# Kernel optimization log

Hardware: AMD Instinct MI355X
Metric: run time of the kernel (lower is better)

Reference implementation:

```python
import jax, jax.numpy as jnp
import numpy as np

B, T, D, H = 2, 2048, 1024, 16
DK = D // H


def setup_inputs() -> dict:
    key = jax.random.key(0)
    ks = jax.random.split(key, 12)
    s = 0.02
    return {
        "query": jax.random.normal(ks[0], (B, T, D), jnp.float32),
        "key": jax.random.normal(ks[1], (B, T, D), jnp.float32),
        "value": jax.random.normal(ks[2], (B, T, D), jnp.float32),
        "mask": jax.random.randint(ks[3], (B, T), 0, 2) != 0,  # True = keep
        "Wq": jax.random.normal(ks[4], (D, D), jnp.float32) * s,
        "bq": jnp.zeros((D,), jnp.float32),
        "Wk": jax.random.normal(ks[5], (D, D), jnp.float32) * s,
        "bk": jnp.zeros((D,), jnp.float32),
        "Wv": jax.random.normal(ks[6], (D, D), jnp.float32) * s,
        "bv": jnp.zeros((D,), jnp.float32),
        "Wo": jax.random.normal(ks[7], (D, D), jnp.float32) * s,
        "bo": jnp.zeros((D,), jnp.float32),
    }


def _split_heads(x):
    # [B, S, D] -> [B, H, S, DK]
    b, s, _ = x.shape
    return x.reshape(b, s, H, DK).transpose(0, 2, 1, 3)


def reference(query, key, value, mask, Wq, bq, Wk, bk, Wv, bv, Wo, bo):
    # torch Linear: y = x @ W.T + b
    q = _split_heads(query @ Wq.T + bq)   # [B,H,T,DK]
    k = _split_heads(key @ Wk.T + bk)     # [B,H,S,DK]
    v = _split_heads(value @ Wv.T + bv)   # [B,H,S,DK]
    scale = 1.0 / np.sqrt(DK).astype(np.float32)
    scores = jnp.einsum('bhtd,bhsd->bhts', q, k) * scale  # [B,H,T,S]
    # key-padding mask [B,S] -> broadcast [B,1,1,S], True = keep
    scores = jnp.where(mask[:, None, None, :], scores, -jnp.inf)
    attn = jax.nn.softmax(scores, axis=-1)
    out = jnp.einsum('bhts,bhsd->bhtd', attn, v)           # [B,H,T,DK]
    out = out.transpose(0, 2, 1, 3).reshape(query.shape[0], -1, D)
    return out @ Wo.T + bo
```

## Files before the change

kernel.cpp:

```cpp
#include <hip/hip_runtime.h>
#include <stdint.h>

#define B_SZ 2
#define T_SEQ 2048
#define DMODEL 1024
#define NHEAD 16
#define DKH 64
#define M_ROWS (B_SZ * T_SEQ)

#define LDT 72

#define INP_E  4194304u
#define W_E    1048576u

typedef __bf16 bf16x8 __attribute__((ext_vector_type(8)));
typedef float  f32x4  __attribute__((ext_vector_type(4)));

__device__ __forceinline__ unsigned short f2bf(float f) {
    unsigned u = __builtin_bit_cast(unsigned, f);
    u += 0x7fffu + ((u >> 16) & 1u);
    return (unsigned short)(u >> 16);
}
__device__ __forceinline__ uint4 cvt8(const float* p) {
    float4 f0 = *(const float4*)p, f1 = *(const float4*)(p + 4);
    uint4 r;
    r.x = (unsigned)f2bf(f0.x) | ((unsigned)f2bf(f0.y) << 16);
    r.y = (unsigned)f2bf(f0.z) | ((unsigned)f2bf(f0.w) << 16);
    r.z = (unsigned)f2bf(f1.x) | ((unsigned)f2bf(f1.y) << 16);
    r.w = (unsigned)f2bf(f1.z) | ((unsigned)f2bf(f1.w) << 16);
    return r;
}

__device__ __forceinline__ void async16(const unsigned short* g, unsigned short* l) {
    __builtin_amdgcn_global_load_lds(
        (const __attribute__((address_space(1))) void*)g,
        (__attribute__((address_space(3))) void*)l, 16, 0, 0);
}

__global__ __launch_bounds__(256) void cvt_all(
    const float* __restrict__ q, const float* __restrict__ k, const float* __restrict__ v,
    const float* __restrict__ wq, const float* __restrict__ wk,
    const float* __restrict__ wv, const float* __restrict__ wo,
    unsigned short* __restrict__ wsb)
{
    int blk = blockIdx.x;
    const float* src; unsigned short* dst; int lb;
    if      (blk < 2048) { src = q;  dst = wsb;                       lb = blk; }
    else if (blk < 4096) { src = k;  dst = wsb + INP_E;               lb = blk - 2048; }
    else if (blk < 6144) { src = v;  dst = wsb + 2 * INP_E;           lb = blk - 4096; }
    else if (blk < 6656) { src = wq; dst = wsb + 3 * INP_E;           lb = blk - 6144; }
    else if (blk < 7168) { src = wk; dst = wsb + 3 * INP_E + W_E;     lb = blk - 6656; }
    else if (blk < 7680) { src = wv; dst = wsb + 3 * INP_E + 2 * W_E; lb = blk - 7168; }
    else                 { src = wo; dst = wsb + 3 * INP_E + 3 * W_E; lb = blk - 7680; }
    size_t i = ((size_t)lb * 256 + threadIdx.x) * 8;
    *(uint4*)&dst[i] = cvt8(src + i);
}

template<int C_MODE>
__device__ __forceinline__ void gemm_core(
    const unsigned short* __restrict__ A, const unsigned short* __restrict__ W,
    const float* __restrict__ bias, void* __restrict__ C,
    int N, int K, int bx, int by,
    unsigned short* sA, unsigned short* sB)
{
    const int tid  = threadIdx.x;
    const int wave = tid >> 6, lane = tid & 63;
    const int quad = lane >> 4, l15 = lane & 15;
    const int m0 = by * 128, n0 = bx * 128;
    const int wm = (wave & 1) * 64, wn = (wave >> 1) * 64;

    f32x4 acc[4][4] = {};

    for (int k0 = 0; k0 < K; k0 += 64) {
        __syncthreads();
        #pragma unroll
        for (int i = 0; i < 4; i++) {
            int c   = tid + 256 * i;
            int row = c >> 3;
            int gk  = ((c & 7) ^ (row & 7)) * 8;
            int sb  = (wave * 64 + 256 * i) * 8;
            async16(&A[(size_t)(m0 + row) * K + k0 + gk], sA + sb);
            async16(&W[(size_t)(n0 + row) * K + k0 + gk], sB + sb);
        }
        __syncthreads();
        #pragma unroll
        for (int ks = 0; ks < 2; ks++) {
            const int sw = l15 & 7;
            bf16x8 af[4], bfv[4];
            #pragma unroll
            for (int mt = 0; mt < 4; mt++)
                af[mt] = *(const bf16x8*)&sA[(wm + mt * 16 + l15) * 64 +
                                             (((ks * 4 + quad) ^ sw) * 8)];
            #pragma unroll
            for (int nt = 0; nt < 4; nt++)
                bfv[nt] = *(const bf16x8*)&sB[(wn + nt * 16 + l15) * 64 +
                                              (((ks * 4 + quad) ^ sw) * 8)];
            #pragma unroll
            for (int mt = 0; mt < 4; mt++)
                #pragma unroll
                for (int nt = 0; nt < 4; nt++)
                    acc[mt][nt] = __builtin_amdgcn_mfma_f32_16x16x32_bf16(
                        af[mt], bfv[nt], acc[mt][nt], 0, 0, 0);
        }
    }

    if (C_MODE == 2) {
        #pragma unroll
        for (int mt = 0; mt < 4; mt++) {
            #pragma unroll
            for (int r = 0; r < 4; r++) {
                int m = m0 + wm + mt * 16 + quad * 4 + r;
                float bm = bias[m];
                #pragma unroll
                for (int nt = 0; nt < 4; nt++) {
                    int n = n0 + wn + nt * 16 + l15;
                    int bb = n >> 11, t = n & 2047;
                    ((unsigned short*)C)[((size_t)bb * 1024 + m) * 2048 + t] =
                        f2bf(acc[mt][nt][r] + bm);
                }
            }
        }
    } else {
        #pragma unroll
        for (int nt = 0; nt < 4; nt++) {
            int n = n0 + wn + nt * 16 + l15;
            float bv = bias[n];
            #pragma unroll
            for (int mt = 0; mt < 4; mt++) {
                #pragma unroll
                for (int r = 0; r < 4; r++) {
                    int m = m0 + wm + mt * 16 + quad * 4 + r;
                    float val = acc[mt][nt][r] + bv;
                    if (C_MODE == 1) ((float*)C)[(size_t)m * N + n] = val;
                    else ((unsigned short*)C)[(size_t)m * N + n] = f2bf(val);
                }
            }
        }
    }
}

__global__ __launch_bounds__(256) void gemm_qkv(
    const unsigned short* __restrict__ Qb, const unsigned short* __restrict__ Kb,
    const unsigned short* __restrict__ Vb,
    const unsigned short* __restrict__ Wqb, const unsigned short* __restrict__ Wkb,
    const unsigned short* __restrict__ Wvb,
    const float* __restrict__ bq, const float* __restrict__ bk, const float* __restrict__ bv,
    unsigned short* __restrict__ Qp, unsigned short* __restrict__ Kp,
    unsigned short* __restrict__ Vt)
{
    __shared__ __align__(16) unsigned short sA[128 * 64];
    __shared__ __align__(16) unsigned short sB[128 * 64];
    const int z = blockIdx.z, id = blockIdx.x;
    if (z < 2) {
        gemm_core<0>(z ? Kb : Qb, z ? Wkb : Wqb, z ? bk : bq, z ? Kp : Qp,
                     DMODEL, DMODEL, id & 7, id >> 3, sA, sB);
    } else {
        gemm_core<2>(Wvb, Vb, bv, Vt, M_ROWS, DMODEL, id & 31, id >> 5, sA, sB);
    }
}

__global__ __launch_bounds__(256) void gemm_o(
    const unsigned short* __restrict__ AO, const unsigned short* __restrict__ Wob,
    const float* __restrict__ bo, float* __restrict__ out)
{
    __shared__ __align__(16) unsigned short sA[128 * 64];
    __shared__ __align__(16) unsigned short sB[128 * 64];
    const int id = blockIdx.x;
    gemm_core<1>(AO, Wob, bo, out, DMODEL, DMODEL, id & 7, id >> 3, sA, sB);
}

template<int A_BF16, int W_BF16, int C_MODE>
__global__ __launch_bounds__(256) void gemm_bt_cvt(
    const void* __restrict__ A_, const void* __restrict__ W_,
    const float* __restrict__ bias, void* __restrict__ C_,
    int M, int N, int K)
{
    __shared__ __align__(16) unsigned short sA[128 * LDT];
    __shared__ __align__(16) unsigned short sB[128 * LDT];
    const int tid  = threadIdx.x;
    const int wave = tid >> 6, lane = tid & 63;
    const int quad = lane >> 4, l15 = lane & 15;
    const int m0 = blockIdx.y * 128, n0 = blockIdx.x * 128;
    const int wm = (wave & 1) * 64, wn = (wave >> 1) * 64;
    f32x4 acc[4][4] = {};
    for (int k0 = 0; k0 < K; k0 += 64) {
        __syncthreads();
        #pragma unroll
        for (int i = 0; i < 4; i++) {
            int c = tid + 256 * i;
            int row = c >> 3, koff = (c & 7) * 8;
            if (A_BF16)
                *(uint4*)&sA[row * LDT + koff] =
                    *(const uint4*)&((const unsigned short*)A_)[(size_t)(m0 + row) * K + k0 + koff];
            else
                *(uint4*)&sA[row * LDT + koff] =
                    cvt8((const float*)A_ + (size_t)(m0 + row) * K + k0 + koff);
            if (W_BF16)
                *(uint4*)&sB[row * LDT + koff] =
                    *(const uint4*)&((const unsigned short*)W_)[(size_t)(n0 + row) * K + k0 + koff];
            else
                *(uint4*)&sB[row * LDT + koff] =
                    cvt8((const float*)W_ + (size_t)(n0 + row) * K + k0 + koff);
        }
        __syncthreads();
        #pragma unroll
        for (int ks = 0; ks < 2; ks++) {
            bf16x8 af[4], bfr[4];
            #pragma unroll
            for (int mt = 0; mt < 4; mt++)
                af[mt] = *(const bf16x8*)&sA[(wm + mt * 16 + l15) * LDT + ks * 32 + quad * 8];
            #pragma unroll
            for (int nt = 0; nt < 4; nt++)
                bfr[nt] = *(const bf16x8*)&sB[(wn + nt * 16 + l15) * LDT + ks * 32 + quad * 8];
            #pragma unroll
            for (int mt = 0; mt < 4; mt++)
                #pragma unroll
                for (int nt = 0; nt < 4; nt++)
                    acc[mt][nt] = __builtin_amdgcn_mfma_f32_16x16x32_bf16(
                        af[mt], bfr[nt], acc[mt][nt], 0, 0, 0);
        }
    }
    if (C_MODE == 2) {
        #pragma unroll
        for (int mt = 0; mt < 4; mt++)
            #pragma unroll
            for (int r = 0; r < 4; r++) {
                int m = m0 + wm + mt * 16 + quad * 4 + r;
                float bm = bias[m];
                #pragma unroll
                for (int nt = 0; nt < 4; nt++) {
                    int n = n0 + wn + nt * 16 + l15;
                    int bb = n >> 11, t = n & 2047;
                    ((unsigned short*)C_)[((size_t)bb * 1024 + m) * 2048 + t] =
                        f2bf(acc[mt][nt][r] + bm);
                }
            }
    } else {
        #pragma unroll
        for (int nt = 0; nt < 4; nt++) {
            int n = n0 + wn + nt * 16 + l15;
            float bv = bias[n];
            #pragma unroll
            for (int mt = 0; mt < 4; mt++)
                #pragma unroll
                for (int r = 0; r < 4; r++) {
                    int m = m0 + wm + mt * 16 + quad * 4 + r;
                    float val = acc[mt][nt][r] + bv;
                    if (C_MODE == 1) ((float*)C_)[(size_t)m * N + n] = val;
                    else ((unsigned short*)C_)[(size_t)m * N + n] = f2bf(val);
                }
        }
    }
}

__global__ __launch_bounds__(256) void attn_kernel(
    const unsigned short* __restrict__ Qp,
    const unsigned short* __restrict__ Kp,
    const unsigned short* __restrict__ Vt,
    const int* __restrict__ maskp,
    unsigned short* __restrict__ Op)
{
    __shared__ __align__(16) unsigned short sK[64 * LDT];
    __shared__ __align__(16) unsigned short sV[64 * LDT];
    __shared__ __align__(16) unsigned short sP[4 * 16 * LDT];
    __shared__ float smask[64];

    const int tid  = threadIdx.x;
    const int wave = tid >> 6, lane = tid & 63;
    const int quad = lane >> 4, l15 = lane & 15;
    const int qblk = blockIdx.x, h = blockIdx.y, b = blockIdx.z;

    const float SCL2 = 0.125f * 1.44269504089f;
    const float MNEG = -30000.f;

    const int qrow = qblk * 64 + wave * 16 + l15;
    const unsigned short* qptr = Qp + (size_t)(b * T_SEQ + qrow) * DMODEL + h * DKH + quad * 8;
    const bf16x8 aq0 = *(const bf16x8*)qptr;
    const bf16x8 aq1 = *(const bf16x8*)(qptr + 32);

    f32x4 O[4] = {};
    float l_r[4] = {0.f, 0.f, 0.f, 0.f};

    unsigned short* sPw = sP + wave * 16 * LDT;
    const unsigned short* VtB = Vt + (size_t)b * DMODEL * T_SEQ + (size_t)h * DKH * T_SEQ;

    for (int s0 = 0; s0 < T_SEQ; s0 += 64) {
        __syncthreads();
        #pragma unroll
        for (int i = 0; i < 2; i++) {
            int c = tid + 256 * i;
            int row = c >> 3, off = (c & 7) * 8;
            *(uint4*)&sK[row * LDT + off] =
                *(const uint4*)&Kp[(size_t)(b * T_SEQ + s0 + row) * DMODEL + h * DKH + off];
            *(uint4*)&sV[row * LDT + off] =
                *(const uint4*)&VtB[(size_t)row * T_SEQ + s0 + off];
        }
        if (tid < 64)
            smask[tid] = maskp[b * T_SEQ + s0 + tid] ? 0.f : MNEG;
        __syncthreads();

        f32x4 S[4];
        #pragma unroll
        for (int nt = 0; nt < 4; nt++) {
            const unsigned short* kb = &sK[(nt * 16 + l15) * LDT + quad * 8];
            f32x4 z = {};
            z = __builtin_amdgcn_mfma_f32_16x16x32_bf16(aq0, *(const bf16x8*)kb, z, 0, 0, 0);
            z = __builtin_amdgcn_mfma_f32_16x16x32_bf16(aq1, *(const bf16x8*)(kb + 32), z, 0, 0, 0);
            S[nt] = z;
        }

        #pragma unroll
        for (int nt = 0; nt < 4; nt++) {
            float madd = smask[nt * 16 + l15];
            #pragma unroll
            for (int r = 0; r < 4; r++) {
                float p = __builtin_amdgcn_exp2f(S[nt][r] * SCL2 + madd);
                l_r[r] += p;
                unsigned u = __builtin_bit_cast(unsigned, p) + 0x8000u;
                sPw[(quad * 4 + r) * LDT + nt * 16 + l15] = (unsigned short)(u >> 16);
            }
        }
        __syncthreads();

        const bf16x8 ap0 = *(const bf16x8*)&sPw[l15 * LDT + quad * 8];
        const bf16x8 ap1 = *(const bf16x8*)&sPw[l15 * LDT + 32 + quad * 8];
        #pragma unroll
        for (int nt = 0; nt < 4; nt++) {
            const unsigned short* vb = &sV[(nt * 16 + l15) * LDT + quad * 8];
            O[nt] = __builtin_amdgcn_mfma_f32_16x16x32_bf16(ap0, *(const bf16x8*)vb, O[nt], 0, 0, 0);
            O[nt] = __builtin_amdgcn_mfma_f32_16x16x32_bf16(ap1, *(const bf16x8*)(vb + 32), O[nt], 0, 0, 0);
        }
    }

    #pragma unroll
    for (int r = 0; r < 4; r++) {
        float l = l_r[r];
        l += __shfl_xor(l, 1);
        l += __shfl_xor(l, 2);
        l += __shfl_xor(l, 4);
        l += __shfl_xor(l, 8);
        l_r[r] = 1.0f / fmaxf(l, 1e-30f);
    }
    #pragma unroll
    for (int nt = 0; nt < 4; nt++) {
        #pragma unroll
        for (int r = 0; r < 4; r++) {
            int q = qblk * 64 + wave * 16 + quad * 4 + r;
            Op[(size_t)(b * T_SEQ + q) * DMODEL + h * DKH + nt * 16 + l15] =
                f2bf(O[nt][r] * l_r[r]);
        }
    }
}

extern "C" void kernel_launch(void* const* d_in, const int* in_sizes, int n_in,
                              void* d_out, int out_size, void* d_ws, size_t ws_size,
                              hipStream_t stream)
{
    const float* q  = (const float*)d_in[0];
    const float* k  = (const float*)d_in[1];
    const float* v  = (const float*)d_in[2];
    const int*   mk = (const int*)d_in[3];
    const float* Wq = (const float*)d_in[4];
    const float* bq = (const float*)d_in[5];
    const float* Wk = (const float*)d_in[6];
    const float* bk = (const float*)d_in[7];
    const float* Wv = (const float*)d_in[8];
    const float* bv = (const float*)d_in[9];
    const float* Wo = (const float*)d_in[10];
    const float* bo = (const float*)d_in[11];
    float* out = (float*)d_out;

    unsigned short* wsb = (unsigned short*)d_ws;
    const dim3 gA(T_SEQ / 64, NHEAD, B_SZ);

    if (ws_size >= (size_t)64 * 1024 * 1024) {
        unsigned short* Qb  = wsb;
        unsigned short* Kb  = wsb + INP_E;
        unsigned short* Vb  = wsb + 2 * INP_E;
        unsigned short* Wqb = wsb + 3 * INP_E;
        unsigned short* Wkb = wsb + 3 * INP_E + W_E;
        unsigned short* Wvb = wsb + 3 * INP_E + 2 * W_E;
        unsigned short* Wob = wsb + 3 * INP_E + 3 * W_E;
        unsigned short* Qp  = wsb + 4 * INP_E;
        unsigned short* Kp  = wsb + 5 * INP_E;
        unsigned short* Vt  = wsb + 6 * INP_E;
        unsigned short* AO  = wsb + 7 * INP_E;

        cvt_all<<<8192, 256, 0, stream>>>(q, k, v, Wq, Wk, Wv, Wo, wsb);
        gemm_qkv<<<dim3(256, 1, 3), 256, 0, stream>>>(
            Qb, Kb, Vb, Wqb, Wkb, Wvb, bq, bk, bv, Qp, Kp, Vt);
        attn_kernel<<<gA, 256, 0, stream>>>(Qp, Kp, Vt, mk, AO);
        gemm_o<<<dim3(256, 1, 1), 256, 0, stream>>>(AO, Wob, bo, out);
    } else {
        unsigned short* Qp = wsb;
        unsigned short* Kp = wsb + INP_E;
        unsigned short* Vt = wsb + 2 * INP_E;
        unsigned short* AO = wsb + 3 * INP_E;
        const dim3 gN(DMODEL / 128, M_ROWS / 128);
        const dim3 gV(M_ROWS / 128, DMODEL / 128);
        gemm_bt_cvt<0, 0, 0><<<gN, 256, 0, stream>>>(q, Wq, bq, Qp, M_ROWS, DMODEL, DMODEL);
        gemm_bt_cvt<0, 0, 0><<<gN, 256, 0, stream>>>(k, Wk, bk, Kp, M_ROWS, DMODEL, DMODEL);
        gemm_bt_cvt<0, 0, 2><<<gV, 256, 0, stream>>>(Wv, v, bv, Vt, DMODEL, M_ROWS, DMODEL);
        attn_kernel<<<gA, 256, 0, stream>>>(Qp, Kp, Vt, mk, AO);
        gemm_bt_cvt<1, 0, 1><<<gN, 256, 0, stream>>>(AO, Wo, bo, out, M_ROWS, DMODEL, DMODEL);
    }
}
```

Baseline: 256.9 us.

## Enlarge attention key tile with register prefetch; halve output GEMM M-tile

Result: slower. 348.3 us (+35.6%).

```diff
diff --git a/kernel.cpp b/kernel.cpp
--- a/kernel.cpp
+++ b/kernel.cpp
@@ -9,6 +9,7 @@
 #define M_ROWS (B_SZ * T_SEQ)
 
 #define LDT 72
+#define LDP 136
 
 #define INP_E  4194304u
 #define W_E    1048576u
@@ -56,7 +57,7 @@
     *(uint4*)&dst[i] = cvt8(src + i);
 }
 
-template<int C_MODE>
+template<int C_MODE, int MT>
 __device__ __forceinline__ void gemm_core(
     const unsigned short* __restrict__ A, const unsigned short* __restrict__ W,
     const float* __restrict__ bias, void* __restrict__ C,
@@ -66,29 +67,37 @@
     const int tid  = threadIdx.x;
     const int wave = tid >> 6, lane = tid & 63;
     const int quad = lane >> 4, l15 = lane & 15;
-    const int m0 = by * 128, n0 = bx * 128;
-    const int wm = (wave & 1) * 64, wn = (wave >> 1) * 64;
-
-    f32x4 acc[4][4] = {};
+    const int TM = MT * 32;
+    const int m0 = by * TM, n0 = bx * 128;
+    const int wm = (wave & 1) * (MT * 16), wn = (wave >> 1) * 64;
+
+    f32x4 acc[MT][4] = {};
 
     for (int k0 = 0; k0 < K; k0 += 64) {
         __syncthreads();
+        #pragma unroll
+        for (int i = 0; i < MT; i++) {
+            int c   = tid + 256 * i;
+            int row = c >> 3;
+            int gk  = ((c & 7) ^ (row & 7)) * 8;
+            int sb  = (wave * 64 + 256 * i) * 8;
+            async16(&A[(size_t)(m0 + row) * K + k0 + gk], sA + sb);
+        }
         #pragma unroll
         for (int i = 0; i < 4; i++) {
             int c   = tid + 256 * i;
             int row = c >> 3;
             int gk  = ((c & 7) ^ (row & 7)) * 8;
             int sb  = (wave * 64 + 256 * i) * 8;
-            async16(&A[(size_t)(m0 + row) * K + k0 + gk], sA + sb);
             async16(&W[(size_t)(n0 + row) * K + k0 + gk], sB + sb);
         }
         __syncthreads();
+        const int sw = l15 & 7;
         #pragma unroll
         for (int ks = 0; ks < 2; ks++) {
-            const int sw = l15 & 7;
-            bf16x8 af[4], bfv[4];
-            #pragma unroll
-            for (int mt = 0; mt < 4; mt++)
+            bf16x8 af[MT], bfv[4];
+            #pragma unroll
+            for (int mt = 0; mt < MT; mt++)
                 af[mt] = *(const bf16x8*)&sA[(wm + mt * 16 + l15) * 64 +
                                              (((ks * 4 + quad) ^ sw) * 8)];
             #pragma unroll
@@ -96,7 +105,7 @@
                 bfv[nt] = *(const bf16x8*)&sB[(wn + nt * 16 + l15) * 64 +
                                               (((ks * 4 + quad) ^ sw) * 8)];
             #pragma unroll
-            for (int mt = 0; mt < 4; mt++)
+            for (int mt = 0; mt < MT; mt++)
                 #pragma unroll
                 for (int nt = 0; nt < 4; nt++)
                     acc[mt][nt] = __builtin_amdgcn_mfma_f32_16x16x32_bf16(
@@ -106,7 +115,7 @@
 
     if (C_MODE == 2) {
         #pragma unroll
-        for (int mt = 0; mt < 4; mt++) {
+        for (int mt = 0; mt < MT; mt++) {
             #pragma unroll
             for (int r = 0; r < 4; r++) {
                 int m = m0 + wm + mt * 16 + quad * 4 + r;
@@ -126,7 +135,7 @@
             int n = n0 + wn + nt * 16 + l15;
             float bv = bias[n];
             #pragma unroll
-            for (int mt = 0; mt < 4; mt++) {
+            for (int mt = 0; mt < MT; mt++) {
                 #pragma unroll
                 for (int r = 0; r < 4; r++) {
                     int m = m0 + wm + mt * 16 + quad * 4 + r;
@@ -152,10 +161,10 @@
     __shared__ __align__(16) unsigned short sB[128 * 64];
     const int z = blockIdx.z, id = blockIdx.x;
     if (z < 2) {
-        gemm_core<0>(z ? Kb : Qb, z ? Wkb : Wqb, z ? bk : bq, z ? Kp : Qp,
-                     DMODEL, DMODEL, id & 7, id >> 3, sA, sB);
+        gemm_core<0, 4>(z ? Kb : Qb, z ? Wkb : Wqb, z ? bk : bq, z ? Kp : Qp,
+                        DMODEL, DMODEL, id & 7, id >> 3, sA, sB);
     } else {
-        gemm_core<2>(Wvb, Vb, bv, Vt, M_ROWS, DMODEL, id & 31, id >> 5, sA, sB);
+        gemm_core<2, 4>(Wvb, Vb, bv, Vt, M_ROWS, DMODEL, id & 31, id >> 5, sA, sB);
     }
 }
 
@@ -163,10 +172,131 @@
     const unsigned short* __restrict__ AO, const unsigned short* __restrict__ Wob,
     const float* __restrict__ bo, float* __restrict__ out)
 {
-    __shared__ __align__(16) unsigned short sA[128 * 64];
+    __shared__ __align__(16) unsigned short sA[64 * 64];
     __shared__ __align__(16) unsigned short sB[128 * 64];
     const int id = blockIdx.x;
-    gemm_core<1>(AO, Wob, bo, out, DMODEL, DMODEL, id & 7, id >> 3, sA, sB);
+    gemm_core<1, 2>(AO, Wob, bo, out, DMODEL, DMODEL, id & 7, id >> 3, sA, sB);
+}
+
+__global__ __launch_bounds__(256) void attn_kernel(
+    const unsigned short* __restrict__ Qp,
+    const unsigned short* __restrict__ Kp,
+    const unsigned short* __restrict__ Vt,
+    const int* __restrict__ maskp,
+    unsigned short* __restrict__ Op)
+{
+    __shared__ __align__(16) unsigned short sK[128 * LDT];
+    __shared__ __align__(16) unsigned short sV[64 * LDP];
+    __shared__ __align__(16) unsigned short sP[4 * 16 * LDP];
+    __shared__ float smask[128];
+
+    const int tid  = threadIdx.x;
+    const int wave = tid >> 6, lane = tid & 63;
+    const int quad = lane >> 4, l15 = lane & 15;
+    const int qblk = blockIdx.x, h = blockIdx.y, b = blockIdx.z;
+
+    const float SCL2 = 0.125f * 1.44269504089f;
+    const float MNEG = -30000.f;
+
+    const int qrow = qblk * 64 + wave * 16 + l15;
+    const unsigned short* qptr = Qp + (size_t)(b * T_SEQ + qrow) * DMODEL + h * DKH + quad * 8;
+    const bf16x8 aq0 = *(const bf16x8*)qptr;
+    const bf16x8 aq1 = *(const bf16x8*)(qptr + 32);
+
+    const unsigned short* Kb_ = Kp + (size_t)b * T_SEQ * DMODEL + h * DKH;
+    const unsigned short* VtB = Vt + ((size_t)b * DMODEL + h * DKH) * T_SEQ;
+
+    f32x4 O[4] = {};
+    float l_r[4] = {0.f, 0.f, 0.f, 0.f};
+    unsigned short* sPw = sP + wave * 16 * LDP;
+
+    int krow[4], koff[4], vrow[4], voff[4];
+    #pragma unroll
+    for (int i = 0; i < 4; i++) {
+        int c = tid + 256 * i;
+        krow[i] = c >> 3;  koff[i] = (c & 7) * 8;
+        vrow[i] = c >> 4;  voff[i] = (c & 15) * 8;
+    }
+
+    uint4 kr[4], vr[4]; int mreg = 0;
+    #pragma unroll
+    for (int i = 0; i < 4; i++) {
+        kr[i] = *(const uint4*)&Kb_[(size_t)krow[i] * DMODEL + koff[i]];
+        vr[i] = *(const uint4*)&VtB[(size_t)vrow[i] * T_SEQ + voff[i]];
+    }
+    if (tid < 128) mreg = maskp[b * T_SEQ + tid];
+
+    for (int it = 0; it < T_SEQ / 128; it++) {
+        const int s0 = it * 128;
+        __syncthreads();
+        #pragma unroll
+        for (int i = 0; i < 4; i++) {
+            *(uint4*)&sK[krow[i] * LDT + koff[i]] = kr[i];
+            *(uint4*)&sV[vrow[i] * LDP + voff[i]] = vr[i];
+        }
+        if (tid < 128) smask[tid] = mreg ? 0.f : MNEG;
+        __syncthreads();
+
+        const int sn = (s0 + 128) & (T_SEQ - 1);
+        #pragma unroll
+        for (int i = 0; i < 4; i++) {
+            kr[i] = *(const uint4*)&Kb_[(size_t)(sn + krow[i]) * DMODEL + koff[i]];
+            vr[i] = *(const uint4*)&VtB[(size_t)vrow[i] * T_SEQ + sn + voff[i]];
+        }
+        if (tid < 128) mreg = maskp[b * T_SEQ + sn + tid];
+
+        f32x4 S[8];
+        #pragma unroll
+        for (int nt = 0; nt < 8; nt++) {
+            const unsigned short* kb = &sK[(nt * 16 + l15) * LDT + quad * 8];
+            f32x4 z = {};
+            z = __builtin_amdgcn_mfma_f32_16x16x32_bf16(aq0, *(const bf16x8*)kb, z, 0, 0, 0);
+            z = __builtin_amdgcn_mfma_f32_16x16x32_bf16(aq1, *(const bf16x8*)(kb + 32), z, 0, 0, 0);
+            S[nt] = z;
+        }
+
+        #pragma unroll
+        for (int nt = 0; nt < 8; nt++) {
+            float madd = smask[nt * 16 + l15];
+            #pragma unroll
+            for (int r = 0; r < 4; r++) {
+                float p = __builtin_amdgcn_exp2f(fmaf(S[nt][r], SCL2, madd));
+                l_r[r] += p;
+                unsigned u = __builtin_bit_cast(unsigned, p) + 0x8000u;
+                sPw[(quad * 4 + r) * LDP + nt * 16 + l15] = (unsigned short)(u >> 16);
+            }
+        }
+        __syncthreads();
+
+        #pragma unroll
+        for (int ksc = 0; ksc < 4; ksc++) {
+            const bf16x8 ap = *(const bf16x8*)&sPw[l15 * LDP + ksc * 32 + quad * 8];
+            #pragma unroll
+            for (int nt = 0; nt < 4; nt++) {
+                const unsigned short* vb = &sV[(nt * 16 + l15) * LDP + ksc * 32 + quad * 8];
+                O[nt] = __builtin_amdgcn_mfma_f32_16x16x32_bf16(ap, *(const bf16x8*)vb, O[nt], 0, 0, 0);
+            }
+        }
+    }
+
+    #pragma unroll
+    for (int r = 0; r < 4; r++) {
+        float l = l_r[r];
+        l += __shfl_xor(l, 1);
+        l += __shfl_xor(l, 2);
+        l += __shfl_xor(l, 4);
+        l += __shfl_xor(l, 8);
+        l_r[r] = 1.0f / fmaxf(l, 1e-30f);
+    }
+    #pragma unroll
+    for (int nt = 0; nt < 4; nt++) {
+        #pragma unroll
+        for (int r = 0; r < 4; r++) {
+            int q = qblk * 64 + wave * 16 + quad * 4 + r;
+            Op[(size_t)(b * T_SEQ + q) * DMODEL + h * DKH + nt * 16 + l15] =
+                f2bf(O[nt][r] * l_r[r]);
+        }
+    }
 }
 
 template<int A_BF16, int W_BF16, int C_MODE>
@@ -253,105 +383,6 @@
     }
 }
 
-__global__ __launch_bounds__(256) void attn_kernel(
-    const unsigned short* __restrict__ Qp,
-    const unsigned short* __restrict__ Kp,
-    const unsigned short* __restrict__ Vt,
-    const int* __restrict__ maskp,
-    unsigned short* __restrict__ Op)
-{
-    __shared__ __align__(16) unsigned short sK[64 * LDT];
-    __shared__ __align__(16) unsigned short sV[64 * LDT];
-    __shared__ __align__(16) unsigned short sP[4 * 16 * LDT];
-    __shared__ float smask[64];
-
-    const int tid  = threadIdx.x;
-    const int wave = tid >> 6, lane = tid & 63;
-    const int quad = lane >> 4, l15 = lane & 15;
-    const int qblk = blockIdx.x, h = blockIdx.y, b = blockIdx.z;
-
-    const float SCL2 = 0.125f * 1.44269504089f;
-    const float MNEG = -30000.f;
-
-    const int qrow = qblk * 64 + wave * 16 + l15;
-    const unsigned short* qptr = Qp + (size_t)(b * T_SEQ + qrow) * DMODEL + h * DKH + quad * 8;
-    const bf16x8 aq0 = *(const bf16x8*)qptr;
-    const bf16x8 aq1 = *(const bf16x8*)(qptr + 32);
-
-    f32x4 O[4] = {};
-    float l_r[4] = {0.f, 0.f, 0.f, 0.f};
-
-    unsigned short* sPw = sP + wave * 16 * LDT;
-    const unsigned short* VtB = Vt + (size_t)b * DMODEL * T_SEQ + (size_t)h * DKH * T_SEQ;
-
-    for (int s0 = 0; s0 < T_SEQ; s0 += 64) {
-        __syncthreads();
-        #pragma unroll
-        for (int i = 0; i < 2; i++) {
-            int c = tid + 256 * i;
-            int row = c >> 3, off = (c & 7) * 8;
-            *(uint4*)&sK[row * LDT + off] =
-                *(const uint4*)&Kp[(size_t)(b * T_SEQ + s0 + row) * DMODEL + h * DKH + off];
-            *(uint4*)&sV[row * LDT + off] =
-                *(const uint4*)&VtB[(size_t)row * T_SEQ + s0 + off];
-        }
-        if (tid < 64)
-            smask[tid] = maskp[b * T_SEQ + s0 + tid] ? 0.f : MNEG;
-        __syncthreads();
-
-        f32x4 S[4];
-        #pragma unroll
-        for (int nt = 0; nt < 4; nt++) {
-            const unsigned short* kb = &sK[(nt * 16 + l15) * LDT + quad * 8];
-            f32x4 z = {};
-            z = __builtin_amdgcn_mfma_f32_16x16x32_bf16(aq0, *(const bf16x8*)kb, z, 0, 0, 0);
-            z = __builtin_amdgcn_mfma_f32_16x16x32_bf16(aq1, *(const bf16x8*)(kb + 32), z, 0, 0, 0);
-            S[nt] = z;
-        }
-
-        #pragma unroll
-        for (int nt = 0; nt < 4; nt++) {
-            float madd = smask[nt * 16 + l15];
-            #pragma unroll
-            for (int r = 0; r < 4; r++) {
-                float p = __builtin_amdgcn_exp2f(S[nt][r] * SCL2 + madd);
-                l_r[r] += p;
-                unsigned u = __builtin_bit_cast(unsigned, p) + 0x8000u;
-                sPw[(quad * 4 + r) * LDT + nt * 16 + l15] = (unsigned short)(u >> 16);
-            }
-        }
-        __syncthreads();
-
-        const bf16x8 ap0 = *(const bf16x8*)&sPw[l15 * LDT + quad * 8];
-        const bf16x8 ap1 = *(const bf16x8*)&sPw[l15 * LDT + 32 + quad * 8];
-        #pragma unroll
-        for (int nt = 0; nt < 4; nt++) {
-            const unsigned short* vb = &sV[(nt * 16 + l15) * LDT + quad * 8];
-            O[nt] = __builtin_amdgcn_mfma_f32_16x16x32_bf16(ap0, *(const bf16x8*)vb, O[nt], 0, 0, 0);
-            O[nt] = __builtin_amdgcn_mfma_f32_16x16x32_bf16(ap1, *(const bf16x8*)(vb + 32), O[nt], 0, 0, 0);
-        }
-    }
-
-    #pragma unroll
-    for (int r = 0; r < 4; r++) {
-        float l = l_r[r];
-        l += __shfl_xor(l, 1);
-        l += __shfl_xor(l, 2);
-        l += __shfl_xor(l, 4);
-        l += __shfl_xor(l, 8);
-        l_r[r] = 1.0f / fmaxf(l, 1e-30f);
-    }
-    #pragma unroll
-    for (int nt = 0; nt < 4; nt++) {
-        #pragma unroll
-        for (int r = 0; r < 4; r++) {
-            int q = qblk * 64 + wave * 16 + quad * 4 + r;
-            Op[(size_t)(b * T_SEQ + q) * DMODEL + h * DKH + nt * 16 + l15] =
-                f2bf(O[nt][r] * l_r[r]);
-        }
-    }
-}
-
 extern "C" void kernel_launch(void* const* d_in, const int* in_sizes, int n_in,
                               void* d_out, int out_size, void* d_ws, size_t ws_size,
                               hipStream_t stream)
@@ -390,7 +421,7 @@
         gemm_qkv<<<dim3(256, 1, 3), 256, 0, stream>>>(
             Qb, Kb, Vb, Wqb, Wkb, Wvb, bq, bk, bv, Qp, Kp, Vt);
         attn_kernel<<<gA, 256, 0, stream>>>(Qp, Kp, Vt, mk, AO);
-        gemm_o<<<dim3(256, 1, 1), 256, 0, stream>>>(AO, Wob, bo, out);
+        gemm_o<<<dim3(512, 1, 1), 256, 0, stream>>>(AO, Wob, bo, out);
     } else {
         unsigned short* Qp = wsb;
         unsigned short* Kp = wsb + INP_E;
```

## Halve gemm_o M-tile and use async swizzled LDS loads in attention

Applied to the files above, without the earlier changes.

Result: faster. 244.1 us (-5.0%).

```diff
diff --git a/kernel.cpp b/kernel.cpp
--- a/kernel.cpp
+++ b/kernel.cpp
@@ -56,7 +56,7 @@
     *(uint4*)&dst[i] = cvt8(src + i);
 }
 
-template<int C_MODE>
+template<int C_MODE, int MT>
 __device__ __forceinline__ void gemm_core(
     const unsigned short* __restrict__ A, const unsigned short* __restrict__ W,
     const float* __restrict__ bias, void* __restrict__ C,
@@ -66,29 +66,37 @@
     const int tid  = threadIdx.x;
     const int wave = tid >> 6, lane = tid & 63;
     const int quad = lane >> 4, l15 = lane & 15;
-    const int m0 = by * 128, n0 = bx * 128;
-    const int wm = (wave & 1) * 64, wn = (wave >> 1) * 64;
-
-    f32x4 acc[4][4] = {};
+    const int TM = MT * 32;
+    const int m0 = by * TM, n0 = bx * 128;
+    const int wm = (wave & 1) * (MT * 16), wn = (wave >> 1) * 64;
+
+    f32x4 acc[MT][4] = {};
 
     for (int k0 = 0; k0 < K; k0 += 64) {
         __syncthreads();
+        #pragma unroll
+        for (int i = 0; i < MT; i++) {
+            int c   = tid + 256 * i;
+            int row = c >> 3;
+            int gk  = ((c & 7) ^ (row & 7)) * 8;
+            int sb  = (wave * 64 + 256 * i) * 8;
+            async16(&A[(size_t)(m0 + row) * K + k0 + gk], sA + sb);
+        }
         #pragma unroll
         for (int i = 0; i < 4; i++) {
             int c   = tid + 256 * i;
             int row = c >> 3;
             int gk  = ((c & 7) ^ (row & 7)) * 8;
             int sb  = (wave * 64 + 256 * i) * 8;
-            async16(&A[(size_t)(m0 + row) * K + k0 + gk], sA + sb);
             async16(&W[(size_t)(n0 + row) * K + k0 + gk], sB + sb);
         }
         __syncthreads();
+        const int sw = l15 & 7;
         #pragma unroll
         for (int ks = 0; ks < 2; ks++) {
-            const int sw = l15 & 7;
-            bf16x8 af[4], bfv[4];
-            #pragma unroll
-            for (int mt = 0; mt < 4; mt++)
+            bf16x8 af[MT], bfv[4];
+            #pragma unroll
+            for (int mt = 0; mt < MT; mt++)
                 af[mt] = *(const bf16x8*)&sA[(wm + mt * 16 + l15) * 64 +
                                              (((ks * 4 + quad) ^ sw) * 8)];
             #pragma unroll
@@ -96,7 +104,7 @@
                 bfv[nt] = *(const bf16x8*)&sB[(wn + nt * 16 + l15) * 64 +
                                               (((ks * 4 + quad) ^ sw) * 8)];
             #pragma unroll
-            for (int mt = 0; mt < 4; mt++)
+            for (int mt = 0; mt < MT; mt++)
                 #pragma unroll
                 for (int nt = 0; nt < 4; nt++)
                     acc[mt][nt] = __builtin_amdgcn_mfma_f32_16x16x32_bf16(
@@ -106,7 +114,7 @@
 
     if (C_MODE == 2) {
         #pragma unroll
-        for (int mt = 0; mt < 4; mt++) {
+        for (int mt = 0; mt < MT; mt++) {
             #pragma unroll
             for (int r = 0; r < 4; r++) {
                 int m = m0 + wm + mt * 16 + quad * 4 + r;
@@ -126,7 +134,7 @@
             int n = n0 + wn + nt * 16 + l15;
             float bv = bias[n];
             #pragma unroll
-            for (int mt = 0; mt < 4; mt++) {
+            for (int mt = 0; mt < MT; mt++) {
                 #pragma unroll
                 for (int r = 0; r < 4; r++) {
                     int m = m0 + wm + mt * 16 + quad * 4 + r;
@@ -152,10 +160,10 @@
     __shared__ __align__(16) unsigned short sB[128 * 64];
     const int z = blockIdx.z, id = blockIdx.x;
     if (z < 2) {
-        gemm_core<0>(z ? Kb : Qb, z ? Wkb : Wqb, z ? bk : bq, z ? Kp : Qp,
-                     DMODEL, DMODEL, id & 7, id >> 3, sA, sB);
+        gemm_core<0, 4>(z ? Kb : Qb, z ? Wkb : Wqb, z ? bk : bq, z ? Kp : Qp,
+                        DMODEL, DMODEL, id & 7, id >> 3, sA, sB);
     } else {
-        gemm_core<2>(Wvb, Vb, bv, Vt, M_ROWS, DMODEL, id & 31, id >> 5, sA, sB);
+        gemm_core<2, 4>(Wvb, Vb, bv, Vt, M_ROWS, DMODEL, id & 31, id >> 5, sA, sB);
     }
 }
 
@@ -163,10 +171,115 @@
     const unsigned short* __restrict__ AO, const unsigned short* __restrict__ Wob,
     const float* __restrict__ bo, float* __restrict__ out)
 {
-    __shared__ __align__(16) unsigned short sA[128 * 64];
+    __shared__ __align__(16) unsigned short sA[64 * 64];
     __shared__ __align__(16) unsigned short sB[128 * 64];
     const int id = blockIdx.x;
-    gemm_core<1>(AO, Wob, bo, out, DMODEL, DMODEL, id & 7, id >> 3, sA, sB);
+    gemm_core<1, 2>(AO, Wob, bo, out, DMODEL, DMODEL, id & 7, id >> 3, sA, sB);
+}
+
+__global__ __launch_bounds__(256) void attn_kernel(
+    const unsigned short* __restrict__ Qp,
+    const unsigned short* __restrict__ Kp,
+    const unsigned short* __restrict__ Vt,
+    const int* __restrict__ maskp,
+    unsigned short* __restrict__ Op)
+{
+    __shared__ __align__(16) unsigned short sK[64 * 64];
+    __shared__ __align__(16) unsigned short sV[64 * 64];
+    __shared__ __align__(16) unsigned short sP[4 * 16 * LDT];
+    __shared__ float smask[64];
+
+    const int tid  = threadIdx.x;
+    const int wave = tid >> 6, lane = tid & 63;
+    const int quad = lane >> 4, l15 = lane & 15;
+    const int qblk = blockIdx.x, h = blockIdx.y, b = blockIdx.z;
+
+    const float SCL2 = 0.125f * 1.44269504089f;
+    const float MNEG = -30000.f;
+
+    const int qrow = qblk * 64 + wave * 16 + l15;
+    const unsigned short* qptr = Qp + (size_t)(b * T_SEQ + qrow) * DMODEL + h * DKH + quad * 8;
+    const bf16x8 aq0 = *(const bf16x8*)qptr;
+    const bf16x8 aq1 = *(const bf16x8*)(qptr + 32);
+
+    const unsigned short* Kb_ = Kp + (size_t)b * T_SEQ * DMODEL + h * DKH;
+    const unsigned short* VtB = Vt + ((size_t)b * DMODEL + h * DKH) * T_SEQ;
+
+    f32x4 O[4] = {};
+    float l_r[4] = {0.f, 0.f, 0.f, 0.f};
+    unsigned short* sPw = sP + wave * 16 * LDT;
+
+    for (int s0 = 0; s0 < T_SEQ; s0 += 64) {
+        __syncthreads();
+        #pragma unroll
+        for (int i = 0; i < 2; i++) {
+            int c   = tid + 256 * i;
+            int row = c >> 3;
+            int gk  = ((c & 7) ^ (row & 7)) * 8;
+            int sb  = (wave * 64 + 256 * i) * 8;
+            async16(&Kb_[(size_t)(s0 + row) * DMODEL + gk], sK + sb);
+            async16(&VtB[(size_t)row * T_SEQ + s0 + gk], sV + sb);
+        }
+        if (tid < 64)
+            smask[tid] = maskp[b * T_SEQ + s0 + tid] ? 0.f : MNEG;
+        __syncthreads();
+
+        const int sw = l15 & 7;
+        f32x4 S[4];
+        #pragma unroll
+        for (int nt = 0; nt < 4; nt++) {
+            const unsigned short* kr = &sK[(nt * 16 + l15) * 64];
+            f32x4 z = {};
+            z = __builtin_amdgcn_mfma_f32_16x16x32_bf16(
+                aq0, *(const bf16x8*)&kr[(quad ^ sw) * 8], z, 0, 0, 0);
+            z = __builtin_amdgcn_mfma_f32_16x16x32_bf16(
+                aq1, *(const bf16x8*)&kr[((quad + 4) ^ sw) * 8], z, 0, 0, 0);
+            S[nt] = z;
+        }
+
+        #pragma unroll
+        for (int nt = 0; nt < 4; nt++) {
+            float madd = smask[nt * 16 + l15];
+            #pragma unroll
+            for (int r = 0; r < 4; r++) {
+                float p = __builtin_amdgcn_exp2f(fmaf(S[nt][r], SCL2, madd));
+                l_r[r] += p;
+                unsigned u = __builtin_bit_cast(unsigned, p) + 0x8000u;
+                sPw[(quad * 4 + r) * LDT + nt * 16 + l15] = (unsigned short)(u >> 16);
+            }
+        }
+        __syncthreads();
+
+        const bf16x8 ap0 = *(const bf16x8*)&sPw[l15 * LDT + quad * 8];
+        const bf16x8 ap1 = *(const bf16x8*)&sPw[l15 * LDT + 32 + quad * 8];
+        #pragma unroll
+        for (int nt = 0; nt < 4; nt++) {
+            const unsigned short* vr = &sV[(nt * 16 + l15) * 64];
+            O[nt] = __builtin_amdgcn_mfma_f32_16x16x32_bf16(
+                ap0, *(const bf16x8*)&vr[(quad ^ sw) * 8], O[nt], 0, 0, 0);
+            O[nt] = __builtin_amdgcn_mfma_f32_16x16x32_bf16(
+                ap1, *(const bf16x8*)&vr[((quad + 4) ^ sw) * 8], O[nt], 0, 0, 0);
+        }
+    }
+
+    #pragma unroll
+    for (int r = 0; r < 4; r++) {
+        float l = l_r[r];
+        l += __shfl_xor(l, 1);
+        l += __shfl_xor(l, 2);
+        l += __shfl_xor(l, 4);
+        l += __shfl_xor(l, 8);
+        l_r[r] = 1.0f / fmaxf(l, 1e-30f);
+    }
+    #pragma unroll
+    for (int nt = 0; nt < 4; nt++) {
+        #pragma unroll
+        for (int r = 0; r < 4; r++) {
+            int q = qblk * 64 + wave * 16 + quad * 4 + r;
+            Op[(size_t)(b * T_SEQ + q) * DMODEL + h * DKH + nt * 16 + l15] =
+                f2bf(O[nt][r] * l_r[r]);
+        }
+    }
 }
 
 template<int A_BF16, int W_BF16, int C_MODE>
@@ -253,105 +366,6 @@
     }
 }
 
-__global__ __launch_bounds__(256) void attn_kernel(
-    const unsigned short* __restrict__ Qp,
-    const unsigned short* __restrict__ Kp,
-    const unsigned short* __restrict__ Vt,
-    const int* __restrict__ maskp,
-    unsigned short* __restrict__ Op)
-{
-    __shared__ __align__(16) unsigned short sK[64 * LDT];
-    __shared__ __align__(16) unsigned short sV[64 * LDT];
-    __shared__ __align__(16) unsigned short sP[4 * 16 * LDT];
-    __shared__ float smask[64];
-
-    const int tid  = threadIdx.x;
-    const int wave = tid >> 6, lane = tid & 63;
-    const int quad = lane >> 4, l15 = lane & 15;
-    const int qblk = blockIdx.x, h = blockIdx.y, b = blockIdx.z;
-
-    const float SCL2 = 0.125f * 1.44269504089f;
-    const float MNEG = -30000.f;
-
-    const int qrow = qblk * 64 + wave * 16 + l15;
-    const unsigned short* qptr = Qp + (size_t)(b * T_SEQ + qrow) * DMODEL + h * DKH + quad * 8;
-    const bf16x8 aq0 = *(const bf16x8*)qptr;
-    const bf16x8 aq1 = *(const bf16x8*)(qptr + 32);
-
-    f32x4 O[4] = {};
-    float l_r[4] = {0.f, 0.f, 0.f, 0.f};
-
-    unsigned short* sPw = sP + wave * 16 * LDT;
-    const unsigned short* VtB = Vt + (size_t)b * DMODEL * T_SEQ + (size_t)h * DKH * T_SEQ;
-
-    for (int s0 = 0; s0 < T_SEQ; s0 += 64) {
-        __syncthreads();
-        #pragma unroll
-        for (int i = 0; i < 2; i++) {
-            int c = tid + 256 * i;
-            int row = c >> 3, off = (c & 7) * 8;
-            *(uint4*)&sK[row * LDT + off] =
-                *(const uint4*)&Kp[(size_t)(b * T_SEQ + s0 + row) * DMODEL + h * DKH + off];
-            *(uint4*)&sV[row * LDT + off] =
-                *(const uint4*)&VtB[(size_t)row * T_SEQ + s0 + off];
-        }
-        if (tid < 64)
-            smask[tid] = maskp[b * T_SEQ + s0 + tid] ? 0.f : MNEG;
-        __syncthreads();
-
-        f32x4 S[4];
-        #pragma unroll
-        for (int nt = 0; nt < 4; nt++) {
-            const unsigned short* kb = &sK[(nt * 16 + l15) * LDT + quad * 8];
-            f32x4 z = {};
-            z = __builtin_amdgcn_mfma_f32_16x16x32_bf16(aq0, *(const bf16x8*)kb, z, 0, 0, 0);
-            z = __builtin_amdgcn_mfma_f32_16x16x32_bf16(aq1, *(const bf16x8*)(kb + 32), z, 0, 0, 0);
-            S[nt] = z;
-        }
-
-        #pragma unroll
-        for (int nt = 0; nt < 4; nt++) {
-            float madd = smask[nt * 16 + l15];
-            #pragma unroll
-            for (int r = 0; r < 4; r++) {
-                float p = __builtin_amdgcn_exp2f(S[nt][r] * SCL2 + madd);
-                l_r[r] += p;
-                unsigned u = __builtin_bit_cast(unsigned, p) + 0x8000u;
-                sPw[(quad * 4 + r) * LDT + nt * 16 + l15] = (unsigned short)(u >> 16);
-            }
-        }
-        __syncthreads();
-
-        const bf16x8 ap0 = *(const bf16x8*)&sPw[l15 * LDT + quad * 8];
-        const bf16x8 ap1 = *(const bf16x8*)&sPw[l15 * LDT + 32 + quad * 8];
-        #pragma unroll
-        for (int nt = 0; nt < 4; nt++) {
-            const unsigned short* vb = &sV[(nt * 16 + l15) * LDT + quad * 8];
-            O[nt] = __builtin_amdgcn_mfma_f32_16x16x32_bf16(ap0, *(const bf16x8*)vb, O[nt], 0, 0, 0);
-            O[nt] = __builtin_amdgcn_mfma_f32_16x16x32_bf16(ap1, *(const bf16x8*)(vb + 32), O[nt], 0, 0, 0);
-        }
-    }
-
-    #pragma unroll
-    for (int r = 0; r < 4; r++) {
-        float l = l_r[r];
-        l += __shfl_xor(l, 1);
-        l += __shfl_xor(l, 2);
-        l += __shfl_xor(l, 4);
-        l += __shfl_xor(l, 8);
-        l_r[r] = 1.0f / fmaxf(l, 1e-30f);
-    }
-    #pragma unroll
-    for (int nt = 0; nt < 4; nt++) {
-        #pragma unroll
-        for (int r = 0; r < 4; r++) {
-            int q = qblk * 64 + wave * 16 + quad * 4 + r;
-            Op[(size_t)(b * T_SEQ + q) * DMODEL + h * DKH + nt * 16 + l15] =
-                f2bf(O[nt][r] * l_r[r]);
-        }
-    }
-}
-
 extern "C" void kernel_launch(void* const* d_in, const int* in_sizes, int n_in,
                               void* d_out, int out_size, void* d_ws, size_t ws_size,
                               hipStream_t stream)
@@ -390,7 +404,7 @@
         gemm_qkv<<<dim3(256, 1, 3), 256, 0, stream>>>(
             Qb, Kb, Vb, Wqb, Wkb, Wvb, bq, bk, bv, Qp, Kp, Vt);
         attn_kernel<<<gA, 256, 0, stream>>>(Qp, Kp, Vt, mk, AO);
-        gemm_o<<<dim3(256, 1, 1), 256, 0, stream>>>(AO, Wob, bo, out);
+        gemm_o<<<dim3(512, 1, 1), 256, 0, stream>>>(AO, Wob, bo, out);
     } else {
         unsigned short* Qp = wsb;
         unsigned short* Kp = wsb + INP_E;
```
